# Performance work log

Hardware: AMD Instinct MI355X
Metric: run time of the kernel (lower is better)

Reference implementation:

```python
import jax, jax.numpy as jnp
import numpy as np

LN_EPS = 1e-5


def _pos_embed_2d(w, h, c, dtype=jnp.float32):
    # matches build_2d_sincos_position_embedding: meshgrid indexing='xy' -> (h, w) grids
    grid_w = jnp.arange(w, dtype=jnp.float32)
    grid_h = jnp.arange(h, dtype=jnp.float32)
    gw, gh = jnp.meshgrid(grid_w, grid_h, indexing='xy')  # each (h, w)
    pos_dim = c // 4
    omega = 1.0 / (10000.0 ** (jnp.arange(pos_dim, dtype=jnp.float32) / pos_dim))
    out_w = gw.reshape(-1, 1) * omega[None]  # (h*w, pos_dim)
    out_h = gh.reshape(-1, 1) * omega[None]
    pe = jnp.concatenate([jnp.sin(out_w), jnp.cos(out_w), jnp.sin(out_h), jnp.cos(out_h)], axis=1)
    return pe.astype(dtype)  # (h*w, c)


def setup_inputs() -> dict:
    key = jax.random.key(0)
    k1, k2 = jax.random.split(key)
    N, C, H, W = 16, 256, 40, 40
    x = jax.random.normal(k1, (N, C, H, W), dtype=jnp.float32)
    ln_w = jnp.ones((C,), dtype=jnp.float32)
    ln_b = jnp.zeros((C,), dtype=jnp.float32)
    qkv_w = jax.random.normal(k2, (3 * C, C), dtype=jnp.float32) * 0.02  # 1x1 conv weight
    qkv_b = jnp.zeros((3 * C,), dtype=jnp.float32)
    gamma = jnp.ones((1,), dtype=jnp.float32)
    return {"x": x, "ln_w": ln_w, "ln_b": ln_b, "qkv_w": qkv_w, "qkv_b": qkv_b, "gamma": gamma}


def reference(x, ln_w, ln_b, qkv_w, qkv_b, gamma):
    N, C, H, W = x.shape
    scale = C ** (-0.5)
    identity = x

    # LayerNorm over channels (computed in NHWC like the torch permute dance)
    xh = jnp.transpose(x, (0, 2, 3, 1))  # (N, H, W, C)
    mu = jnp.mean(xh, axis=-1, keepdims=True)
    var = jnp.mean(jnp.square(xh - mu), axis=-1, keepdims=True)
    xn = (xh - mu) * jax.lax.rsqrt(var + LN_EPS) * ln_w + ln_b

    # 1x1 conv == per-pixel linear
    qkv = jnp.einsum('nhwc,oc->nhwo', xn, qkv_w) + qkv_b  # (N, H, W, 3C)
    qkv = qkv.reshape(N, H * W, 3 * C)
    q, k, v = jnp.split(qkv, 3, axis=-1)  # each (N, HW, C)

    pe = _pos_embed_2d(W, H, C, x.dtype)  # (HW, C)
    q = q + pe
    k = k + pe

    attn = jax.nn.softmax(jnp.einsum('nqc,nkc->nqk', q, k) * scale, axis=-1)
    out = jnp.einsum('nqk,nkc->nqc', attn, v)  # (N, HW, C)
    out = jnp.transpose(out, (0, 2, 1)).reshape(N, C, H, W)
    return identity + gamma[0] * out
```

## Files before the change

kernel.cpp:

```cpp
#include <hip/hip_runtime.h>
#include <hip/hip_bf16.h>

typedef float f32x4 __attribute__((ext_vector_type(4)));
typedef float f32x16 __attribute__((ext_vector_type(16)));
typedef __bf16 v8bf __attribute__((ext_vector_type(8)));
typedef unsigned short ushortx4 __attribute__((ext_vector_type(4)));
typedef unsigned short ushortx8 __attribute__((ext_vector_type(8)));
typedef unsigned int uint4v __attribute__((ext_vector_type(4)));

#define NIMG 16
#define CCH  256
#define HWP  1600

#define QSCALE 0.09016844f
#define DEFER_THR 2.885390f

__device__ __forceinline__ unsigned short f2bf(float f) {
  unsigned int u = __builtin_bit_cast(unsigned int, f);
  u = (u + 0x7FFFu + ((u >> 16) & 1u)) >> 16;
  return (unsigned short)u;
}

__device__ __forceinline__ f32x4 mfma16(v8bf a, v8bf b, f32x4 c) {
  return __builtin_amdgcn_mfma_f32_16x16x32_bf16(a, b, c, 0, 0, 0);
}

__device__ __forceinline__ unsigned cvtpk(float a, float b) {
  unsigned r;
  asm("v_cvt_pk_bf16_f32 %0, %1, %2" : "=v"(r) : "v"(a), "v"(b));
  return r;
}
__device__ __forceinline__ float exp2v(float x) {
  float r;
  asm("v_exp_f32 %0, %1" : "=v"(r) : "v"(x));
  return r;
}
__device__ __forceinline__ float sin2pi(float rev) {
  float r;
  asm("v_fract_f32 %0, %1\n\tv_sin_f32 %0, %0" : "=v"(r) : "v"(rev));
  return r;
}
#define PSWAP(a, b) asm("v_permlane32_swap_b32 %0, %1" : "+v"(a), "+v"(b))

__global__ void prep_kernel(const float* __restrict__ qkv_w,
                            float* __restrict__ pe,
                            unsigned short* __restrict__ w_frag) {
  int tid = blockIdx.x * blockDim.x + threadIdx.x;
  int nthr = gridDim.x * blockDim.x;
  for (int i = tid; i < 768 * 256; i += nthr) {
    int o = i >> 8, c = i & 255;
    int tile = o >> 4, lr = o & 15;
    int ks = c >> 5, lg = (c >> 3) & 3, e = c & 7;
    w_frag[(((size_t)tile * 8 + ks) * 64 + lg * 16 + lr) * 8 + e] = f2bf(qkv_w[i]);
  }
  const float oc = 0.20762051f;
  const float inv2pi = 0.15915494f;
  for (int i = tid; i < HWP * 256; i += nthr) {
    int p = i >> 8, c = i & 255;
    int j = p % 40, ii = p / 40;
    int tt = c & 63;
    float omega = exp2v(-(float)tt * oc) * inv2pi;
    float coord = (c < 128) ? (float)j : (float)ii;
    float rev = coord * omega;
    if (c & 64) rev += 0.25f;
    pe[i] = sin2pi(rev);
  }
}

__global__ __launch_bounds__(512, 4) void ln_qkv_kernel(
    const float* __restrict__ x, const float* __restrict__ ln_w, const float* __restrict__ ln_b,
    const unsigned short* __restrict__ w_frag, const float* __restrict__ qkv_b,
    const float* __restrict__ pe,
    unsigned short* __restrict__ q_arr, unsigned short* __restrict__ k_arr,
    unsigned short* __restrict__ v_arr) {
  __shared__ unsigned short bufraw[18432];
  __shared__ float red_s[8][64], red_q[8][64];
  __shared__ float mu_s[64], rs_s[64];

  int t = threadIdx.x;
  int n = blockIdx.x / 25, pt = blockIdx.x % 25;
  int pix0 = pt * 64;
  int p = t & 63, g = t >> 6;
  const float* xb = x + (size_t)n * CCH * HWP + pix0;

  {
    float sum = 0.f, sq = 0.f;
#pragma unroll
    for (int i = 0; i < 32; ++i) {
      float v = xb[(size_t)(g * 32 + i) * HWP + p];
      sum += v; sq += v * v;
    }
    red_s[g][p] = sum; red_q[g][p] = sq;
  }
  __syncthreads();
  if (t < 64) {
    float s = 0.f, q2 = 0.f;
#pragma unroll
    for (int gg = 0; gg < 8; ++gg) { s += red_s[gg][t]; q2 += red_q[gg][t]; }
    float mu = s * (1.f / 256.f);
    float var = q2 * (1.f / 256.f) - mu * mu;
    mu_s[t] = mu;
    rs_s[t] = rsqrtf(var + 1e-5f);
  }
  __syncthreads();
  {
    float mu = mu_s[p], rs = rs_s[p];
    int p7 = p & 7;
#pragma unroll
    for (int i4 = 0; i4 < 8; ++i4) {
      int c0 = g * 32 + i4 * 4;
      f32x4 lw = *(const f32x4*)&ln_w[c0];
      f32x4 lb = *(const f32x4*)&ln_b[c0];
      ushortx4 pk;
#pragma unroll
      for (int r = 0; r < 4; ++r) {
        float v = xb[(size_t)(c0 + r) * HWP + p];
        pk[r] = f2bf((v - mu) * rs * lw[r] + lb[r]);
      }
      int unit = (c0 >> 3) ^ p7;
      *(ushortx4*)&bufraw[p * 256 + unit * 8 + (i4 & 1) * 4] = pk;
    }
  }
  __syncthreads();

  int w = t >> 6, l = t & 63, lr = l & 15, lg = l >> 4;
  int lr7 = lr & 7;
  f32x4 acc[6][4];
#pragma unroll
  for (int nf = 0; nf < 6; ++nf)
#pragma unroll
    for (int mi = 0; mi < 4; ++mi) acc[nf][mi] = (f32x4){0.f, 0.f, 0.f, 0.f};

#pragma unroll
  for (int ks = 0; ks < 8; ++ks) {
    v8bf bF[4];
#pragma unroll
    for (int mi = 0; mi < 4; ++mi)
      bF[mi] = *(const v8bf*)&bufraw[(mi * 16 + lr) * 256 + (((ks * 4 + lg) ^ lr7) * 8)];
#pragma unroll
    for (int nf = 0; nf < 6; ++nf) {
      int tile = w + nf * 8;
      v8bf wf = *(const v8bf*)&w_frag[(((size_t)tile * 8 + ks) * 64 + l) * 8];
#pragma unroll
      for (int mi = 0; mi < 4; ++mi) acc[nf][mi] = mfma16(wf, bF[mi], acc[nf][mi]);
    }
  }
  __syncthreads();

  int lgh = lg >> 1, lgl = lg & 1;

#pragma unroll
  for (int nf = 4; nf < 6; ++nf) {
    int tile = w + nf * 8;
    f32x4 bi = *(const f32x4*)&qkv_b[tile * 16 + lg * 4];
    int chb = (nf - 4) * 16 + lg * 4;
#pragma unroll
    for (int mi = 0; mi < 4; ++mi) {
      int pixl = mi * 16 + lr;
      f32x4 vv = acc[nf][mi] + bi;
#pragma unroll
      for (int r = 0; r < 4; ++r)
        bufraw[(w * 32 + chb + r) * 72 + pixl] = f2bf(vv[r]);
    }
  }

#pragma unroll
  for (int nf = 0; nf < 2; ++nf) {
    int tile = w + nf * 8;
    f32x4 bi = *(const f32x4*)&qkv_b[tile * 16 + lg * 4];
#pragma unroll
    for (int mi = 0; mi < 4; ++mi) {
      int pix = pix0 + mi * 16 + lr;
      f32x4 pev = *(const f32x4*)&pe[(size_t)pix * 256 + tile * 16 + lg * 4];
      f32x4 vv = (acc[nf][mi] + bi + pev) * QSCALE;
      ushortx4 pk = {f2bf(vv[0]), f2bf(vv[1]), f2bf(vv[2]), f2bf(vv[3])};
      int qt = pix >> 5, l31 = pix & 31;
      size_t ad = ((((size_t)n * 50 + qt) * 16 + tile) * 2 + lgh) * 256 + l31 * 8 + lgl * 4;
      *(ushortx4*)&q_arr[ad] = pk;
    }
  }
#pragma unroll
  for (int nf = 2; nf < 4; ++nf) {
    int tile = w + nf * 8;
    int dt = tile - 16;
    f32x4 bi = *(const f32x4*)&qkv_b[tile * 16 + lg * 4];
#pragma unroll
    for (int mi = 0; mi < 4; ++mi) {
      int pix = pix0 + mi * 16 + lr;
      f32x4 pev = *(const f32x4*)&pe[(size_t)pix * 256 + dt * 16 + lg * 4];
      f32x4 vv = acc[nf][mi] + bi + pev;
      ushortx4 pk = {f2bf(vv[0]), f2bf(vv[1]), f2bf(vv[2]), f2bf(vv[3])};
      size_t ad = (((size_t)n * 16 + dt) * 1600 + pix) * 16 + lgh * 8 + lgl * 4;
      *(ushortx4*)&k_arr[ad] = pk;
    }
  }

#pragma unroll
  for (int c = 0; c < 4; ++c) {
    int ch = l & 31;
    int pg = (l >> 5) + c * 2;
    ushortx8 vv = *(const ushortx8*)&bufraw[(w * 32 + ch) * 72 + pg * 8];
    int kvsl = pg >> 1, hi2 = pg & 1;
    int d = (ch & 15) + w * 16 + (ch >> 4) * 128;
    size_t di = (((size_t)n * 100 + pt * 4 + kvsl) * 2 + hi2) * 256 + d;
    *(ushortx8*)&v_arr[di * 8] = vv;
  }
}

__global__ __launch_bounds__(128, 2) void attn_kernel(
    const unsigned short* __restrict__ q_arr, const unsigned short* __restrict__ k_arr,
    const unsigned short* __restrict__ v_arr, const float* __restrict__ x,
    const float* __restrict__ gamma, float* __restrict__ out) {
  __shared__ float sx[4][2][4][64][4];

  int t = threadIdx.x;
  int wv = t >> 6, l = t & 63;
  int l31 = l & 31, hi = l >> 5;
  int dto = wv * 8;
  int dto32 = wv * 4;
  int slot = blockIdx.x & 7, j = blockIdx.x >> 3;
  int n = slot + 8 * (j / 50);
  int qt = j % 50;
  int q0 = qt * 32;

  v8bf qf[8];
  {
    const unsigned short* qp = q_arr + (((size_t)n * 50 + qt) * 32 + hi) * 256 + l31 * 8;
#pragma unroll
    for (int i = 0; i < 8; ++i)
      qf[i] = *(const v8bf*)(qp + (dto + i) * 512);
  }

  f32x16 acc[4];
#pragma unroll
  for (int dd = 0; dd < 4; ++dd)
#pragma unroll
    for (int r = 0; r < 16; ++r) acc[dd][r] = 0.f;

  float m_run = -1e30f, l_run = 0.f;

  const unsigned short* kbase = k_arr + (size_t)n * (16 * 1600 * 16) +
                                (size_t)dto * 25600 + hi * 8;
  const unsigned short* vbase = v_arr + (size_t)n * (100 * 2 * 256 * 8) +
                                hi * 2048 + l31 * 8 + dto32 * 256;

  v8bf kc[8];
#pragma unroll
  for (int i = 0; i < 8; ++i)
    kc[i] = *(const v8bf*)(kbase + (size_t)i * 25600 + l31 * 16);

  f32x16 sA, sB;
#pragma unroll
  for (int r = 0; r < 16; ++r) sA[r] = 0.f;
#pragma unroll
  for (int i = 0; i < 8; ++i)
    sA = __builtin_amdgcn_mfma_f32_32x32x16_bf16(kc[i], qf[i], sA, 0, 0, 0);

#pragma unroll
  for (int r4 = 0; r4 < 4; ++r4) {
    f32x4 vv = {sA[r4 * 4 + 0], sA[r4 * 4 + 1], sA[r4 * 4 + 2], sA[r4 * 4 + 3]};
    *(f32x4*)&sx[0][wv][r4][l][0] = vv;
  }
#pragma unroll
  for (int i = 0; i < 8; ++i)
    kc[i] = *(const v8bf*)(kbase + (size_t)i * 25600 + (32 + l31) * 16);

  v8bf vf0[4], vf1[4];
#pragma unroll
  for (int i = 0; i < 4; ++i) vf0[i] = *(const v8bf*)(vbase + i * 256);
#pragma unroll
  for (int i = 0; i < 4; ++i) vf1[i] = *(const v8bf*)(vbase + 4096 + i * 256);

  auto body = [&](int kt, f32x16& scur, f32x16& snxt, bool nexttile) {
    asm volatile("s_waitcnt lgkmcnt(0)" ::: "memory");
    __builtin_amdgcn_s_barrier();
    int br = kt & 3;
    float p[16];
#pragma unroll
    for (int r4 = 0; r4 < 4; ++r4) {
      f32x4 oth = *(const f32x4*)&sx[br][wv ^ 1][r4][l][0];
#pragma unroll
      for (int rr = 0; rr < 4; ++rr)
        p[r4 * 4 + rr] = scur[r4 * 4 + rr] + oth[rr];
    }
    if (nexttile) {
#pragma unroll
      for (int r = 0; r < 16; ++r) snxt[r] = 0.f;
#pragma unroll
      for (int i = 0; i < 4; ++i)
        snxt = __builtin_amdgcn_mfma_f32_32x32x16_bf16(kc[i], qf[i], snxt, 0, 0, 0);
    }
    float t0 = fmaxf(p[0], p[1]), t1 = fmaxf(p[2], p[3]);
    float t2 = fmaxf(p[4], p[5]), t3 = fmaxf(p[6], p[7]);
    float t4 = fmaxf(p[8], p[9]), t5 = fmaxf(p[10], p[11]);
    float t6 = fmaxf(p[12], p[13]), t7 = fmaxf(p[14], p[15]);
    float mx = fmaxf(fmaxf(fmaxf(t0, t1), fmaxf(t2, t3)),
                     fmaxf(fmaxf(t4, t5), fmaxf(t6, t7)));
    mx = fmaxf(mx, __shfl_xor(mx, 32));
    if (!__all(mx <= m_run + DEFER_THR)) {
      float mnew = fmaxf(m_run, mx);
      float alpha = exp2v(m_run - mnew);
      l_run *= alpha;
#pragma unroll
      for (int dd = 0; dd < 4; ++dd)
#pragma unroll
        for (int r = 0; r < 16; ++r) acc[dd][r] *= alpha;
      m_run = mnew;
    }
    if (nexttile) {
#pragma unroll
      for (int i = 4; i < 8; ++i)
        snxt = __builtin_amdgcn_mfma_f32_32x32x16_bf16(kc[i], qf[i], snxt, 0, 0, 0);
    }
#pragma unroll
    for (int r = 0; r < 16; ++r) p[r] = exp2v(p[r] - m_run);
    float sSum = ((p[0] + p[1]) + (p[2] + p[3])) + ((p[4] + p[5]) + (p[6] + p[7])) +
                 (((p[8] + p[9]) + (p[10] + p[11])) + ((p[12] + p[13]) + (p[14] + p[15])));
    sSum += __shfl_xor(sSum, 32);
    l_run += sSum;

    unsigned x0 = cvtpk(p[0], p[1]), x1 = cvtpk(p[2], p[3]);
    unsigned y0 = cvtpk(p[4], p[5]), y1 = cvtpk(p[6], p[7]);
    PSWAP(x0, y0); PSWAP(x1, y1);
    uint4v u0 = {x0, x1, y0, y1};
    v8bf pf0 = __builtin_bit_cast(v8bf, u0);
    unsigned z0 = cvtpk(p[8], p[9]), z1 = cvtpk(p[10], p[11]);
    unsigned w0 = cvtpk(p[12], p[13]), w1 = cvtpk(p[14], p[15]);
    PSWAP(z0, w0); PSWAP(z1, w1);
    uint4v u1 = {z0, z1, w0, w1};
    v8bf pf1 = __builtin_bit_cast(v8bf, u1);

#pragma unroll
    for (int dd = 0; dd < 4; ++dd) {
      acc[dd] = __builtin_amdgcn_mfma_f32_32x32x16_bf16(vf0[dd], pf0, acc[dd], 0, 0, 0);
      acc[dd] = __builtin_amdgcn_mfma_f32_32x32x16_bf16(vf1[dd], pf1, acc[dd], 0, 0, 0);
    }

    if (nexttile) {
      int bw = (kt + 1) & 3;
#pragma unroll
      for (int r4 = 0; r4 < 4; ++r4) {
        f32x4 vv = {snxt[r4 * 4 + 0], snxt[r4 * 4 + 1], snxt[r4 * 4 + 2], snxt[r4 * 4 + 3]};
        *(f32x4*)&sx[bw][wv][r4][l][0] = vv;
      }
      int kt2 = (kt + 2 < 50) ? kt + 2 : 0;
#pragma unroll
      for (int i = 0; i < 8; ++i)
        kc[i] = *(const v8bf*)(kbase + (size_t)i * 25600 + (kt2 * 32 + l31) * 16);
      const unsigned short* vp = vbase + (size_t)(kt + 1) * 8192;
#pragma unroll
      for (int i = 0; i < 4; ++i) vf0[i] = *(const v8bf*)(vp + i * 256);
#pragma unroll
      for (int i = 0; i < 4; ++i) vf1[i] = *(const v8bf*)(vp + 4096 + i * 256);
    }
  };

  for (int kt = 0; kt < 48; kt += 2) {
    body(kt, sA, sB, true);
    body(kt + 1, sB, sA, true);
  }
  body(48, sA, sB, true);
  body(49, sB, sA, false);

  float inv = 1.f / l_run;
  float gm = gamma[0];
#pragma unroll
  for (int dd = 0; dd < 4; ++dd) {
#pragma unroll
    for (int r = 0; r < 16; ++r) {
      int d = (dto32 + dd) * 32 + (r & 3) + 8 * (r >> 2) + 4 * hi;
      size_t base = ((size_t)n * 256 + d) * HWP + q0 + l31;
      out[base] = x[base] + gm * acc[dd][r] * inv;
    }
  }
}

extern "C" void kernel_launch(void* const* d_in, const int* in_sizes, int n_in,
                              void* d_out, int out_size, void* d_ws, size_t ws_size,
                              hipStream_t stream) {
  const float* x     = (const float*)d_in[0];
  const float* ln_w  = (const float*)d_in[1];
  const float* ln_b  = (const float*)d_in[2];
  const float* qkv_w = (const float*)d_in[3];
  const float* qkv_b = (const float*)d_in[4];
  const float* gamma = (const float*)d_in[5];
  float* out = (float*)d_out;

  char* ws = (char*)d_ws;
  unsigned short* w_frag = (unsigned short*)ws;
  float*          pe     = (float*)(ws + 393216);
  unsigned short* q_arr  = (unsigned short*)(ws + 2031616);
  unsigned short* k_arr  = (unsigned short*)(ws + 15138816);
  unsigned short* v_arr  = (unsigned short*)(ws + 28246016);

  hipLaunchKernelGGL(prep_kernel, dim3(1024), dim3(256), 0, stream, qkv_w, pe, w_frag);
  hipLaunchKernelGGL(ln_qkv_kernel, dim3(400), dim3(512), 0, stream,
                     x, ln_w, ln_b, w_frag, qkv_b, pe, q_arr, k_arr, v_arr);
  hipLaunchKernelGGL(attn_kernel, dim3(800), dim3(128), 0, stream,
                     q_arr, k_arr, v_arr, x, gamma, out);
}
```

Baseline: 118.7 us.

## Pipeline QK scores two tiles ahead with one barrier per two tiles

The attention main loop now handles two key tiles per iteration with one barrier instead of one per tile. Both waves write their partial QK sums to shared memory and each reads both partials, so no wave keeps its own score in registers. The QK accumulation is split into two independent MFMA chains (s0/s1) to shorten the dependency latency, and V fragments are double-buffered (vA/vB) so loads overlap the PV MFMAs. The cost is higher register pressure from the extra accumulator and V buffers, plus more LDS reads per tile.

```diff
diff --git a/kernel.cpp b/kernel.cpp
--- a/kernel.cpp
+++ b/kernel.cpp
@@ -23,6 +23,9 @@
 
 __device__ __forceinline__ f32x4 mfma16(v8bf a, v8bf b, f32x4 c) {
   return __builtin_amdgcn_mfma_f32_16x16x32_bf16(a, b, c, 0, 0, 0);
+}
+__device__ __forceinline__ f32x16 mfma32(v8bf a, v8bf b, f32x16 c) {
+  return __builtin_amdgcn_mfma_f32_32x32x16_bf16(a, b, c, 0, 0, 0);
 }
 
 __device__ __forceinline__ unsigned cvtpk(float a, float b) {
@@ -211,7 +214,7 @@
     const unsigned short* __restrict__ q_arr, const unsigned short* __restrict__ k_arr,
     const unsigned short* __restrict__ v_arr, const float* __restrict__ x,
     const float* __restrict__ gamma, float* __restrict__ out) {
-  __shared__ float sx[4][2][4][64][4];
+  __shared__ float sx[2][2][2][4][64][4];
 
   int t = threadIdx.x;
   int wv = t >> 6, l = t & 63;
@@ -245,122 +248,194 @@
                                 hi * 2048 + l31 * 8 + dto32 * 256;
 
   v8bf kc[8];
-#pragma unroll
-  for (int i = 0; i < 8; ++i)
-    kc[i] = *(const v8bf*)(kbase + (size_t)i * 25600 + l31 * 16);
-
-  f32x16 sA, sB;
-#pragma unroll
-  for (int r = 0; r < 16; ++r) sA[r] = 0.f;
-#pragma unroll
-  for (int i = 0; i < 8; ++i)
-    sA = __builtin_amdgcn_mfma_f32_32x32x16_bf16(kc[i], qf[i], sA, 0, 0, 0);
-
-#pragma unroll
-  for (int r4 = 0; r4 < 4; ++r4) {
-    f32x4 vv = {sA[r4 * 4 + 0], sA[r4 * 4 + 1], sA[r4 * 4 + 2], sA[r4 * 4 + 3]};
-    *(f32x4*)&sx[0][wv][r4][l][0] = vv;
-  }
-#pragma unroll
-  for (int i = 0; i < 8; ++i)
-    kc[i] = *(const v8bf*)(kbase + (size_t)i * 25600 + (32 + l31) * 16);
-
-  v8bf vf0[4], vf1[4];
-#pragma unroll
-  for (int i = 0; i < 4; ++i) vf0[i] = *(const v8bf*)(vbase + i * 256);
-#pragma unroll
-  for (int i = 0; i < 4; ++i) vf1[i] = *(const v8bf*)(vbase + 4096 + i * 256);
-
-  auto body = [&](int kt, f32x16& scur, f32x16& snxt, bool nexttile) {
+  f32x16 s0, s1;
+
+#define LOADK(TT)                                                              \
+  {                                                                            \
+    _Pragma("unroll")                                                          \
+    for (int i = 0; i < 8; ++i)                                                \
+      kc[i] = *(const v8bf*)(kbase + (size_t)i * 25600 + ((TT) * 32 + l31) * 16); \
+  }
+#define QKFULL()                                                               \
+  {                                                                            \
+    _Pragma("unroll")                                                          \
+    for (int r = 0; r < 16; ++r) { s0[r] = 0.f; s1[r] = 0.f; }                 \
+    _Pragma("unroll")                                                          \
+    for (int i = 0; i < 8; i += 2) {                                           \
+      s0 = mfma32(kc[i], qf[i], s0);                                           \
+      s1 = mfma32(kc[i + 1], qf[i + 1], s1);                                   \
+    }                                                                          \
+  }
+#define WRS(SL, TI)                                                            \
+  {                                                                            \
+    _Pragma("unroll")                                                          \
+    for (int r4 = 0; r4 < 4; ++r4) {                                           \
+      f32x4 vv = {s0[r4 * 4 + 0] + s1[r4 * 4 + 0], s0[r4 * 4 + 1] + s1[r4 * 4 + 1], \
+                  s0[r4 * 4 + 2] + s1[r4 * 4 + 2], s0[r4 * 4 + 3] + s1[r4 * 4 + 3]}; \
+      *(f32x4*)&sx[SL][TI][wv][r4][l][0] = vv;                                 \
+    }                                                                          \
+  }
+
+  LOADK(0); QKFULL(); WRS(0, 0);
+  LOADK(1); QKFULL(); WRS(0, 1);
+  LOADK(2);
+  v8bf vA0[4], vA1[4], vB0[4], vB1[4];
+#pragma unroll
+  for (int i = 0; i < 4; ++i) vA0[i] = *(const v8bf*)(vbase + i * 256);
+#pragma unroll
+  for (int i = 0; i < 4; ++i) vA1[i] = *(const v8bf*)(vbase + 4096 + i * 256);
+
+  for (int it = 0; it < 25; ++it) {
+    int s = it & 1;
+    bool more = (it < 24);
     asm volatile("s_waitcnt lgkmcnt(0)" ::: "memory");
     __builtin_amdgcn_s_barrier();
-    int br = kt & 3;
+
     float p[16];
 #pragma unroll
     for (int r4 = 0; r4 < 4; ++r4) {
-      f32x4 oth = *(const f32x4*)&sx[br][wv ^ 1][r4][l][0];
-#pragma unroll
-      for (int rr = 0; rr < 4; ++rr)
-        p[r4 * 4 + rr] = scur[r4 * 4 + rr] + oth[rr];
-    }
-    if (nexttile) {
-#pragma unroll
-      for (int r = 0; r < 16; ++r) snxt[r] = 0.f;
-#pragma unroll
-      for (int i = 0; i < 4; ++i)
-        snxt = __builtin_amdgcn_mfma_f32_32x32x16_bf16(kc[i], qf[i], snxt, 0, 0, 0);
-    }
-    float t0 = fmaxf(p[0], p[1]), t1 = fmaxf(p[2], p[3]);
-    float t2 = fmaxf(p[4], p[5]), t3 = fmaxf(p[6], p[7]);
-    float t4 = fmaxf(p[8], p[9]), t5 = fmaxf(p[10], p[11]);
-    float t6 = fmaxf(p[12], p[13]), t7 = fmaxf(p[14], p[15]);
-    float mx = fmaxf(fmaxf(fmaxf(t0, t1), fmaxf(t2, t3)),
-                     fmaxf(fmaxf(t4, t5), fmaxf(t6, t7)));
-    mx = fmaxf(mx, __shfl_xor(mx, 32));
-    if (!__all(mx <= m_run + DEFER_THR)) {
-      float mnew = fmaxf(m_run, mx);
-      float alpha = exp2v(m_run - mnew);
-      l_run *= alpha;
-#pragma unroll
-      for (int dd = 0; dd < 4; ++dd)
-#pragma unroll
-        for (int r = 0; r < 16; ++r) acc[dd][r] *= alpha;
-      m_run = mnew;
-    }
-    if (nexttile) {
-#pragma unroll
-      for (int i = 4; i < 8; ++i)
-        snxt = __builtin_amdgcn_mfma_f32_32x32x16_bf16(kc[i], qf[i], snxt, 0, 0, 0);
+      f32x4 a = *(const f32x4*)&sx[s][0][0][r4][l][0];
+      f32x4 b = *(const f32x4*)&sx[s][0][1][r4][l][0];
+#pragma unroll
+      for (int rr = 0; rr < 4; ++rr) p[r4 * 4 + rr] = a[rr] + b[rr];
+    }
+    if (more) {
+#pragma unroll
+      for (int r = 0; r < 16; ++r) { s0[r] = 0.f; s1[r] = 0.f; }
+      s0 = mfma32(kc[0], qf[0], s0); s1 = mfma32(kc[1], qf[1], s1);
+      s0 = mfma32(kc[2], qf[2], s0); s1 = mfma32(kc[3], qf[3], s1);
+    }
+    {
+      float t0 = fmaxf(p[0], p[1]), t1 = fmaxf(p[2], p[3]);
+      float t2 = fmaxf(p[4], p[5]), t3 = fmaxf(p[6], p[7]);
+      float t4 = fmaxf(p[8], p[9]), t5 = fmaxf(p[10], p[11]);
+      float t6 = fmaxf(p[12], p[13]), t7 = fmaxf(p[14], p[15]);
+      float mx = fmaxf(fmaxf(fmaxf(t0, t1), fmaxf(t2, t3)),
+                       fmaxf(fmaxf(t4, t5), fmaxf(t6, t7)));
+      mx = fmaxf(mx, __shfl_xor(mx, 32));
+      if (!__all(mx <= m_run + DEFER_THR)) {
+        float mnew = fmaxf(m_run, mx);
+        float alpha = exp2v(m_run - mnew);
+        l_run *= alpha;
+#pragma unroll
+        for (int dd = 0; dd < 4; ++dd)
+#pragma unroll
+          for (int r = 0; r < 16; ++r) acc[dd][r] *= alpha;
+        m_run = mnew;
+      }
+    }
+    if (more) {
+      s0 = mfma32(kc[4], qf[4], s0); s1 = mfma32(kc[5], qf[5], s1);
+      s0 = mfma32(kc[6], qf[6], s0); s1 = mfma32(kc[7], qf[7], s1);
+      WRS(s ^ 1, 0);
+      LOADK(2 * it + 3);
     }
 #pragma unroll
     for (int r = 0; r < 16; ++r) p[r] = exp2v(p[r] - m_run);
-    float sSum = ((p[0] + p[1]) + (p[2] + p[3])) + ((p[4] + p[5]) + (p[6] + p[7])) +
-                 (((p[8] + p[9]) + (p[10] + p[11])) + ((p[12] + p[13]) + (p[14] + p[15])));
-    sSum += __shfl_xor(sSum, 32);
-    l_run += sSum;
-
-    unsigned x0 = cvtpk(p[0], p[1]), x1 = cvtpk(p[2], p[3]);
-    unsigned y0 = cvtpk(p[4], p[5]), y1 = cvtpk(p[6], p[7]);
-    PSWAP(x0, y0); PSWAP(x1, y1);
-    uint4v u0 = {x0, x1, y0, y1};
-    v8bf pf0 = __builtin_bit_cast(v8bf, u0);
-    unsigned z0 = cvtpk(p[8], p[9]), z1 = cvtpk(p[10], p[11]);
-    unsigned w0 = cvtpk(p[12], p[13]), w1 = cvtpk(p[14], p[15]);
-    PSWAP(z0, w0); PSWAP(z1, w1);
-    uint4v u1 = {z0, z1, w0, w1};
-    v8bf pf1 = __builtin_bit_cast(v8bf, u1);
-
-#pragma unroll
-    for (int dd = 0; dd < 4; ++dd) {
-      acc[dd] = __builtin_amdgcn_mfma_f32_32x32x16_bf16(vf0[dd], pf0, acc[dd], 0, 0, 0);
-      acc[dd] = __builtin_amdgcn_mfma_f32_32x32x16_bf16(vf1[dd], pf1, acc[dd], 0, 0, 0);
-    }
-
-    if (nexttile) {
-      int bw = (kt + 1) & 3;
-#pragma unroll
-      for (int r4 = 0; r4 < 4; ++r4) {
-        f32x4 vv = {snxt[r4 * 4 + 0], snxt[r4 * 4 + 1], snxt[r4 * 4 + 2], snxt[r4 * 4 + 3]};
-        *(f32x4*)&sx[bw][wv][r4][l][0] = vv;
+    {
+      float sSum = ((p[0] + p[1]) + (p[2] + p[3])) + ((p[4] + p[5]) + (p[6] + p[7])) +
+                   (((p[8] + p[9]) + (p[10] + p[11])) + ((p[12] + p[13]) + (p[14] + p[15])));
+      sSum += __shfl_xor(sSum, 32);
+      l_run += sSum;
+    }
+    {
+      unsigned x0 = cvtpk(p[0], p[1]), x1 = cvtpk(p[2], p[3]);
+      unsigned y0 = cvtpk(p[4], p[5]), y1 = cvtpk(p[6], p[7]);
+      PSWAP(x0, y0); PSWAP(x1, y1);
+      uint4v u0 = {x0, x1, y0, y1};
+      v8bf pf0 = __builtin_bit_cast(v8bf, u0);
+      unsigned z0 = cvtpk(p[8], p[9]), z1 = cvtpk(p[10], p[11]);
+      unsigned w0 = cvtpk(p[12], p[13]), w1 = cvtpk(p[14], p[15]);
+      PSWAP(z0, w0); PSWAP(z1, w1);
+      uint4v u1 = {z0, z1, w0, w1};
+      v8bf pf1 = __builtin_bit_cast(v8bf, u1);
+      acc[0] = mfma32(vA0[0], pf0, acc[0]); acc[1] = mfma32(vA0[1], pf0, acc[1]);
+      acc[2] = mfma32(vA0[2], pf0, acc[2]); acc[3] = mfma32(vA0[3], pf0, acc[3]);
+      acc[0] = mfma32(vA1[0], pf1, acc[0]); acc[1] = mfma32(vA1[1], pf1, acc[1]);
+      acc[2] = mfma32(vA1[2], pf1, acc[2]); acc[3] = mfma32(vA1[3], pf1, acc[3]);
+    }
+    {
+      const unsigned short* vp = vbase + (size_t)(2 * it + 1) * 8192;
+#pragma unroll
+      for (int i = 0; i < 4; ++i) vB0[i] = *(const v8bf*)(vp + i * 256);
+#pragma unroll
+      for (int i = 0; i < 4; ++i) vB1[i] = *(const v8bf*)(vp + 4096 + i * 256);
+    }
+
+#pragma unroll
+    for (int r4 = 0; r4 < 4; ++r4) {
+      f32x4 a = *(const f32x4*)&sx[s][1][0][r4][l][0];
+      f32x4 b = *(const f32x4*)&sx[s][1][1][r4][l][0];
+#pragma unroll
+      for (int rr = 0; rr < 4; ++rr) p[r4 * 4 + rr] = a[rr] + b[rr];
+    }
+    if (more) {
+#pragma unroll
+      for (int r = 0; r < 16; ++r) { s0[r] = 0.f; s1[r] = 0.f; }
+      s0 = mfma32(kc[0], qf[0], s0); s1 = mfma32(kc[1], qf[1], s1);
+      s0 = mfma32(kc[2], qf[2], s0); s1 = mfma32(kc[3], qf[3], s1);
+    }
+    {
+      float t0 = fmaxf(p[0], p[1]), t1 = fmaxf(p[2], p[3]);
+      float t2 = fmaxf(p[4], p[5]), t3 = fmaxf(p[6], p[7]);
+      float t4 = fmaxf(p[8], p[9]), t5 = fmaxf(p[10], p[11]);
+      float t6 = fmaxf(p[12], p[13]), t7 = fmaxf(p[14], p[15]);
+      float mx = fmaxf(fmaxf(fmaxf(t0, t1), fmaxf(t2, t3)),
+                       fmaxf(fmaxf(t4, t5), fmaxf(t6, t7)));
+      mx = fmaxf(mx, __shfl_xor(mx, 32));
+      if (!__all(mx <= m_run + DEFER_THR)) {
+        float mnew = fmaxf(m_run, mx);
+        float alpha = exp2v(m_run - mnew);
+        l_run *= alpha;
+#pragma unroll
+        for (int dd = 0; dd < 4; ++dd)
+#pragma unroll
+          for (int r = 0; r < 16; ++r) acc[dd][r] *= alpha;
+        m_run = mnew;
       }
-      int kt2 = (kt + 2 < 50) ? kt + 2 : 0;
-#pragma unroll
-      for (int i = 0; i < 8; ++i)
-        kc[i] = *(const v8bf*)(kbase + (size_t)i * 25600 + (kt2 * 32 + l31) * 16);
-      const unsigned short* vp = vbase + (size_t)(kt + 1) * 8192;
-#pragma unroll
-      for (int i = 0; i < 4; ++i) vf0[i] = *(const v8bf*)(vp + i * 256);
-#pragma unroll
-      for (int i = 0; i < 4; ++i) vf1[i] = *(const v8bf*)(vp + 4096 + i * 256);
-    }
-  };
-
-  for (int kt = 0; kt < 48; kt += 2) {
-    body(kt, sA, sB, true);
-    body(kt + 1, sB, sA, true);
-  }
-  body(48, sA, sB, true);
-  body(49, sB, sA, false);
+    }
+    if (more) {
+      s0 = mfma32(kc[4], qf[4], s0); s1 = mfma32(kc[5], qf[5], s1);
+      s0 = mfma32(kc[6], qf[6], s0); s1 = mfma32(kc[7], qf[7], s1);
+      WRS(s ^ 1, 1);
+      int knB = (2 * it + 4 < 50) ? 2 * it + 4 : 0;
+      LOADK(knB);
+    }
+#pragma unroll
+    for (int r = 0; r < 16; ++r) p[r] = exp2v(p[r] - m_run);
+    {
+      float sSum = ((p[0] + p[1]) + (p[2] + p[3])) + ((p[4] + p[5]) + (p[6] + p[7])) +
+                   (((p[8] + p[9]) + (p[10] + p[11])) + ((p[12] + p[13]) + (p[14] + p[15])));
+      sSum += __shfl_xor(sSum, 32);
+      l_run += sSum;
+    }
+    {
+      unsigned x0 = cvtpk(p[0], p[1]), x1 = cvtpk(p[2], p[3]);
+      unsigned y0 = cvtpk(p[4], p[5]), y1 = cvtpk(p[6], p[7]);
+      PSWAP(x0, y0); PSWAP(x1, y1);
+      uint4v u0 = {x0, x1, y0, y1};
+      v8bf pf0 = __builtin_bit_cast(v8bf, u0);
+      unsigned z0 = cvtpk(p[8], p[9]), z1 = cvtpk(p[10], p[11]);
+      unsigned w0 = cvtpk(p[12], p[13]), w1 = cvtpk(p[14], p[15]);
+      PSWAP(z0, w0); PSWAP(z1, w1);
+      uint4v u1 = {z0, z1, w0, w1};
+      v8bf pf1 = __builtin_bit_cast(v8bf, u1);
+      acc[0] = mfma32(vB0[0], pf0, acc[0]); acc[1] = mfma32(vB0[1], pf0, acc[1]);
+      acc[2] = mfma32(vB0[2], pf0, acc[2]); acc[3] = mfma32(vB0[3], pf0, acc[3]);
+      acc[0] = mfma32(vB1[0], pf1, acc[0]); acc[1] = mfma32(vB1[1], pf1, acc[1]);
+      acc[2] = mfma32(vB1[2], pf1, acc[2]); acc[3] = mfma32(vB1[3], pf1, acc[3]);
+    }
+    if (more) {
+      const unsigned short* vp = vbase + (size_t)(2 * it + 2) * 8192;
+#pragma unroll
+      for (int i = 0; i < 4; ++i) vA0[i] = *(const v8bf*)(vp + i * 256);
+#pragma unroll
+      for (int i = 0; i < 4; ++i) vA1[i] = *(const v8bf*)(vp + 4096 + i * 256);
+    }
+  }
+#undef LOADK
+#undef QKFULL
+#undef WRS
 
   float inv = 1.f / l_run;
   float gm = gamma[0];
```

Measured after the change: 118.3 us. About the same (-0.3%).

## Split attention KV range across two wave pairs with flash-decoding style merge

Applied to the files above, without the earlier changes.

Doubles the attention block to four waves, with each pair of waves handling half of the 50 key tiles, and merges the partial softmax states (max, sum, accumulators) through shared memory at the end. The aim is more parallelism per query tile and a shorter serial KV loop, which hides latency better with 800 blocks. In exchange it adds a merge step, extra LDS traffic and barriers, and every launched block now uses more registers and threads, which may lower occupancy.

```diff
diff --git a/kernel.cpp b/kernel.cpp
--- a/kernel.cpp
+++ b/kernel.cpp
@@ -23,6 +23,9 @@
 
 __device__ __forceinline__ f32x4 mfma16(v8bf a, v8bf b, f32x4 c) {
   return __builtin_amdgcn_mfma_f32_16x16x32_bf16(a, b, c, 0, 0, 0);
+}
+__device__ __forceinline__ f32x16 mfma32(v8bf a, v8bf b, f32x16 c) {
+  return __builtin_amdgcn_mfma_f32_32x32x16_bf16(a, b, c, 0, 0, 0);
 }
 
 __device__ __forceinline__ unsigned cvtpk(float a, float b) {
@@ -207,21 +210,24 @@
   }
 }
 
-__global__ __launch_bounds__(128, 2) void attn_kernel(
+__global__ __launch_bounds__(256, 2) void attn_kernel(
     const unsigned short* __restrict__ q_arr, const unsigned short* __restrict__ k_arr,
     const unsigned short* __restrict__ v_arr, const float* __restrict__ x,
     const float* __restrict__ gamma, float* __restrict__ out) {
-  __shared__ float sx[4][2][4][64][4];
+  __shared__ float sx[2][2][2][4][64][4];
+  __shared__ float mls[2][2][2][32];
 
   int t = threadIdx.x;
   int wv = t >> 6, l = t & 63;
   int l31 = l & 31, hi = l >> 5;
-  int dto = wv * 8;
-  int dto32 = wv * 4;
+  int dh = wv & 1, kvh = wv >> 1;
+  int dto = dh * 8;
+  int dto32 = dh * 4;
   int slot = blockIdx.x & 7, j = blockIdx.x >> 3;
   int n = slot + 8 * (j / 50);
   int qt = j % 50;
   int q0 = qt * 32;
+  int kt0 = kvh * 25;
 
   v8bf qf[8];
   {
@@ -247,38 +253,38 @@
   v8bf kc[8];
 #pragma unroll
   for (int i = 0; i < 8; ++i)
-    kc[i] = *(const v8bf*)(kbase + (size_t)i * 25600 + l31 * 16);
+    kc[i] = *(const v8bf*)(kbase + (size_t)i * 25600 + (kt0 * 32 + l31) * 16);
 
   f32x16 sA, sB;
 #pragma unroll
   for (int r = 0; r < 16; ++r) sA[r] = 0.f;
 #pragma unroll
   for (int i = 0; i < 8; ++i)
-    sA = __builtin_amdgcn_mfma_f32_32x32x16_bf16(kc[i], qf[i], sA, 0, 0, 0);
+    sA = mfma32(kc[i], qf[i], sA);
 
 #pragma unroll
   for (int r4 = 0; r4 < 4; ++r4) {
     f32x4 vv = {sA[r4 * 4 + 0], sA[r4 * 4 + 1], sA[r4 * 4 + 2], sA[r4 * 4 + 3]};
-    *(f32x4*)&sx[0][wv][r4][l][0] = vv;
+    *(f32x4*)&sx[0][kvh][dh][r4][l][0] = vv;
   }
 #pragma unroll
   for (int i = 0; i < 8; ++i)
-    kc[i] = *(const v8bf*)(kbase + (size_t)i * 25600 + (32 + l31) * 16);
+    kc[i] = *(const v8bf*)(kbase + (size_t)i * 25600 + ((kt0 + 1) * 32 + l31) * 16);
 
   v8bf vf0[4], vf1[4];
 #pragma unroll
-  for (int i = 0; i < 4; ++i) vf0[i] = *(const v8bf*)(vbase + i * 256);
-#pragma unroll
-  for (int i = 0; i < 4; ++i) vf1[i] = *(const v8bf*)(vbase + 4096 + i * 256);
+  for (int i = 0; i < 4; ++i) vf0[i] = *(const v8bf*)(vbase + (size_t)kt0 * 8192 + i * 256);
+#pragma unroll
+  for (int i = 0; i < 4; ++i) vf1[i] = *(const v8bf*)(vbase + (size_t)kt0 * 8192 + 4096 + i * 256);
 
   auto body = [&](int kt, f32x16& scur, f32x16& snxt, bool nexttile) {
     asm volatile("s_waitcnt lgkmcnt(0)" ::: "memory");
     __builtin_amdgcn_s_barrier();
-    int br = kt & 3;
+    int br = kt & 1;
     float p[16];
 #pragma unroll
     for (int r4 = 0; r4 < 4; ++r4) {
-      f32x4 oth = *(const f32x4*)&sx[br][wv ^ 1][r4][l][0];
+      f32x4 oth = *(const f32x4*)&sx[br][kvh][dh ^ 1][r4][l][0];
 #pragma unroll
       for (int rr = 0; rr < 4; ++rr)
         p[r4 * 4 + rr] = scur[r4 * 4 + rr] + oth[rr];
@@ -288,7 +294,7 @@
       for (int r = 0; r < 16; ++r) snxt[r] = 0.f;
 #pragma unroll
       for (int i = 0; i < 4; ++i)
-        snxt = __builtin_amdgcn_mfma_f32_32x32x16_bf16(kc[i], qf[i], snxt, 0, 0, 0);
+        snxt = mfma32(kc[i], qf[i], snxt);
     }
     float t0 = fmaxf(p[0], p[1]), t1 = fmaxf(p[2], p[3]);
     float t2 = fmaxf(p[4], p[5]), t3 = fmaxf(p[6], p[7]);
@@ -310,7 +316,7 @@
     if (nexttile) {
 #pragma unroll
       for (int i = 4; i < 8; ++i)
-        snxt = __builtin_amdgcn_mfma_f32_32x32x16_bf16(kc[i], qf[i], snxt, 0, 0, 0);
+        snxt = mfma32(kc[i], qf[i], snxt);
     }
 #pragma unroll
     for (int r = 0; r < 16; ++r) p[r] = exp2v(p[r] - m_run);
@@ -332,22 +338,22 @@
 
 #pragma unroll
     for (int dd = 0; dd < 4; ++dd) {
-      acc[dd] = __builtin_amdgcn_mfma_f32_32x32x16_bf16(vf0[dd], pf0, acc[dd], 0, 0, 0);
-      acc[dd] = __builtin_amdgcn_mfma_f32_32x32x16_bf16(vf1[dd], pf1, acc[dd], 0, 0, 0);
+      acc[dd] = mfma32(vf0[dd], pf0, acc[dd]);
+      acc[dd] = mfma32(vf1[dd], pf1, acc[dd]);
     }
 
     if (nexttile) {
-      int bw = (kt + 1) & 3;
+      int bw = (kt + 1) & 1;
 #pragma unroll
       for (int r4 = 0; r4 < 4; ++r4) {
         f32x4 vv = {snxt[r4 * 4 + 0], snxt[r4 * 4 + 1], snxt[r4 * 4 + 2], snxt[r4 * 4 + 3]};
-        *(f32x4*)&sx[bw][wv][r4][l][0] = vv;
+        *(f32x4*)&sx[bw][kvh][dh][r4][l][0] = vv;
       }
-      int kt2 = (kt + 2 < 50) ? kt + 2 : 0;
+      int kt2 = (kt + 2 < 25) ? kt0 + kt + 2 : kt0;
 #pragma unroll
       for (int i = 0; i < 8; ++i)
         kc[i] = *(const v8bf*)(kbase + (size_t)i * 25600 + (kt2 * 32 + l31) * 16);
-      const unsigned short* vp = vbase + (size_t)(kt + 1) * 8192;
+      const unsigned short* vp = vbase + (size_t)(kt0 + kt + 1) * 8192;
 #pragma unroll
       for (int i = 0; i < 4; ++i) vf0[i] = *(const v8bf*)(vp + i * 256);
 #pragma unroll
@@ -355,24 +361,67 @@
     }
   };
 
-  for (int kt = 0; kt < 48; kt += 2) {
+  for (int kt = 0; kt < 24; kt += 2) {
     body(kt, sA, sB, true);
     body(kt + 1, sB, sA, true);
   }
-  body(48, sA, sB, true);
-  body(49, sB, sA, false);
-
-  float inv = 1.f / l_run;
+  body(24, sA, sB, false);
+
+  __syncthreads();
+  if (hi == 0) {
+    mls[kvh][dh][0][l31] = m_run;
+    mls[kvh][dh][1][l31] = l_run;
+  }
+  float* pool = (float*)sx;
+  if (kvh == 0) {
+#pragma unroll
+    for (int r4 = 0; r4 < 4; ++r4) {
+      f32x4 a2 = {acc[2][r4 * 4 + 0], acc[2][r4 * 4 + 1], acc[2][r4 * 4 + 2], acc[2][r4 * 4 + 3]};
+      f32x4 a3 = {acc[3][r4 * 4 + 0], acc[3][r4 * 4 + 1], acc[3][r4 * 4 + 2], acc[3][r4 * 4 + 3]};
+      *(f32x4*)&pool[((0 * 2 + dh) * 2 + 0) * 1024 + r4 * 256 + l * 4] = a2;
+      *(f32x4*)&pool[((0 * 2 + dh) * 2 + 1) * 1024 + r4 * 256 + l * 4] = a3;
+    }
+  } else {
+#pragma unroll
+    for (int r4 = 0; r4 < 4; ++r4) {
+      f32x4 a0 = {acc[0][r4 * 4 + 0], acc[0][r4 * 4 + 1], acc[0][r4 * 4 + 2], acc[0][r4 * 4 + 3]};
+      f32x4 a1 = {acc[1][r4 * 4 + 0], acc[1][r4 * 4 + 1], acc[1][r4 * 4 + 2], acc[1][r4 * 4 + 3]};
+      *(f32x4*)&pool[((1 * 2 + dh) * 2 + 0) * 1024 + r4 * 256 + l * 4] = a0;
+      *(f32x4*)&pool[((1 * 2 + dh) * 2 + 1) * 1024 + r4 * 256 + l * 4] = a1;
+    }
+  }
+  __syncthreads();
+
+  float m_p = mls[kvh ^ 1][dh][0][l31];
+  float l_p = mls[kvh ^ 1][dh][1][l31];
+  float M = fmaxf(m_run, m_p);
+  float a_s = exp2v(m_run - M), a_o = exp2v(m_p - M);
+  float linv = 1.f / (l_run * a_s + l_p * a_o);
   float gm = gamma[0];
-#pragma unroll
-  for (int dd = 0; dd < 4; ++dd) {
-#pragma unroll
-    for (int r = 0; r < 16; ++r) {
-      int d = (dto32 + dd) * 32 + (r & 3) + 8 * (r >> 2) + 4 * hi;
-      size_t base = ((size_t)n * 256 + d) * HWP + q0 + l31;
-      out[base] = x[base] + gm * acc[dd][r] * inv;
-    }
-  }
+
+#define FIN(DT, RG)                                                             \
+  {                                                                             \
+    _Pragma("unroll")                                                           \
+    for (int r4 = 0; r4 < 4; ++r4) {                                            \
+      f32x4 oth = *(const f32x4*)&pool[(RG) * 1024 + r4 * 256 + l * 4];         \
+      _Pragma("unroll")                                                         \
+      for (int rr = 0; rr < 4; ++rr) {                                          \
+        int r = r4 * 4 + rr;                                                    \
+        float o = acc[DT][r] * a_s + oth[rr] * a_o;                             \
+        int d = (dto32 + (DT)) * 32 + (r & 3) + 8 * (r >> 2) + 4 * hi;          \
+        size_t base = ((size_t)n * 256 + d) * HWP + q0 + l31;                   \
+        out[base] = x[base] + gm * o * linv;                                    \
+      }                                                                         \
+    }                                                                           \
+  }
+  if (kvh == 0) {
+    FIN(0, (1 * 2 + dh) * 2 + 0);
+    FIN(1, (1 * 2 + dh) * 2 + 1);
+  } else {
+    FIN(2, (0 * 2 + dh) * 2 + 0);
+    FIN(3, (0 * 2 + dh) * 2 + 1);
+  }
+#undef FIN
 }
 
 extern "C" void kernel_launch(void* const* d_in, const int* in_sizes, int n_in,
@@ -396,6 +445,6 @@
   hipLaunchKernelGGL(prep_kernel, dim3(1024), dim3(256), 0, stream, qkv_w, pe, w_frag);
   hipLaunchKernelGGL(ln_qkv_kernel, dim3(400), dim3(512), 0, stream,
                      x, ln_w, ln_b, w_frag, qkv_b, pe, q_arr, k_arr, v_arr);
-  hipLaunchKernelGGL(attn_kernel, dim3(800), dim3(128), 0, stream,
+  hipLaunchKernelGGL(attn_kernel, dim3(800), dim3(256), 0, stream,
                      q_arr, k_arr, v_arr, x, gamma, out);
 }
```

New measurement: 126.6 us. 1.07x slower.
